# Performance work log

Hardware: AMD Instinct MI355X
Metric: run time of the kernel (lower is better)

Reference implementation:

```python
import jax, jax.numpy as jnp
import numpy as np

B, S, E, H = 2, 2048, 1024, 16
D = E // H  # head_dim = 64


def setup_inputs() -> dict:
    key = jax.random.key(0)
    k1, k2, k3 = jax.random.split(key, 3)
    scale = 0.02  # GPT-2 init scale
    return {
        "hidden_states": jax.random.normal(k1, (B, S, E), dtype=jnp.float32),
        "c_attn_w": jax.random.normal(k2, (E, 3 * E), dtype=jnp.float32) * scale,
        "c_attn_b": jnp.zeros((3 * E,), dtype=jnp.float32),
        "c_proj_w": jax.random.normal(k3, (E, E), dtype=jnp.float32) * scale,
        "c_proj_b": jnp.zeros((E,), dtype=jnp.float32),
    }


def reference(hidden_states, c_attn_w, c_attn_b, c_proj_w, c_proj_b):
    # Conv1D: x @ W + b  -> qkv [B, S, 3E]
    qkv = hidden_states @ c_attn_w + c_attn_b
    q, k, v = jnp.split(qkv, 3, axis=-1)

    # split heads -> [B, H, S, D]
    def split_heads(t):
        return t.reshape(B, S, H, D).transpose(0, 2, 1, 3)

    q, k, v = split_heads(q), split_heads(k), split_heads(v)

    # naive full attention: QK^T / sqrt(D) -> softmax -> @ V
    attn_weights = jnp.einsum("bhqd,bhkd->bhqk", q, k) / jnp.sqrt(
        jnp.asarray(D, dtype=q.dtype)
    )
    attn_weights = jax.nn.softmax(attn_weights, axis=-1)
    attn_output = jnp.einsum("bhqk,bhkd->bhqd", attn_weights, v)

    # merge heads -> [B, S, E], then output projection
    attn_output = attn_output.transpose(0, 2, 1, 3).reshape(B, S, E)
    attn_output = attn_output @ c_proj_w + c_proj_b
    return attn_output
```

## Files before the change

### kernel.cpp

```cpp
#include <hip/hip_runtime.h>

#define SEQ 2048
#define EMB 1024
#define KDIM 1024
#define CF 0.180336880111113f

typedef __attribute__((ext_vector_type(8))) short short8_t;
typedef __attribute__((ext_vector_type(4))) float floatx4;
typedef __attribute__((ext_vector_type(4))) unsigned short ushort4_t;
typedef __attribute__((ext_vector_type(4))) unsigned int uivec4;

#define GLOAD16(gp, lp)                                                        \
  __builtin_amdgcn_global_load_lds(                                            \
      (const __attribute__((address_space(1))) void*)(gp),                     \
      (__attribute__((address_space(3))) void*)(lp), 16, 0, 0)

#define WGBAR()                                   \
  do {                                            \
    __asm__ __volatile__("" ::: "memory");        \
    __builtin_amdgcn_s_barrier();                 \
    __asm__ __volatile__("" ::: "memory");        \
  } while (0)

static __device__ __forceinline__ unsigned short f2bf(float x) {
  unsigned int u = __float_as_uint(x);
  return (unsigned short)((u + 0x7fffu + ((u >> 16) & 1u)) >> 16);
}

static __device__ __forceinline__ short8_t mk_pb(unsigned int a, unsigned int b,
                                                 unsigned int c, unsigned int d) {
  uivec4 t;
  t[0] = a; t[1] = b; t[2] = c; t[3] = d;
  return __builtin_bit_cast(short8_t, t);
}

static __device__ __forceinline__ unsigned int pack_bf(float p0, float p1) {
  return __builtin_amdgcn_perm(__float_as_uint(p1), __float_as_uint(p0),
                               0x07060302u);
}

static __device__ __forceinline__ void tconv_tile(
    const float* __restrict__ W, unsigned short* __restrict__ T, int N, int K,
    int n0, int k0, int tid) {
  __shared__ float Tl[64][65];
  const int lx = tid & 15, ly = tid >> 4;
#pragma unroll
  for (int u = 0; u < 4; ++u) {
    int r = u * 16 + ly;
    float4 v = *(const float4*)&W[(size_t)(k0 + r) * N + n0 + lx * 4];
    Tl[r][lx * 4 + 0] = v.x;
    Tl[r][lx * 4 + 1] = v.y;
    Tl[r][lx * 4 + 2] = v.z;
    Tl[r][lx * 4 + 3] = v.w;
  }
  __syncthreads();
#pragma unroll
  for (int u = 0; u < 4; ++u) {
    int n = u * 16 + ly;
    ushort4_t h;
#pragma unroll
    for (int v = 0; v < 4; ++v) h[v] = f2bf(Tl[lx * 4 + v][n]);
    *(ushort4_t*)&T[(size_t)(n0 + n) * K + k0 + lx * 4] = h;
  }
}

__global__ __launch_bounds__(256) void prep(
    const float* __restrict__ hs, const float* __restrict__ caw,
    const float* __restrict__ cpw, unsigned short* __restrict__ hsb,
    unsigned short* __restrict__ w1t, unsigned short* __restrict__ w2t) {
  const int bid = blockIdx.x, tid = threadIdx.x;
  if (bid < 4096) {
    const int i = bid * 256 + tid;
    float4 v = *(const float4*)&hs[(size_t)i * 4];
    ushort4_t h = {f2bf(v.x), f2bf(v.y), f2bf(v.z), f2bf(v.w)};
    *(ushort4_t*)&hsb[(size_t)i * 4] = h;
  } else if (bid < 4864) {
    const int idx = bid - 4096;
    tconv_tile(caw, w1t, 3 * EMB, EMB, (idx % 48) * 64, (idx / 48) * 64, tid);
  } else {
    const int idx = bid - 4864;
    tconv_tile(cpw, w2t, EMB, EMB, (idx % 16) * 64, (idx / 16) * 64, tid);
  }
}

template <int MODE, int BN>
__global__ __launch_bounds__(256, 4) void gemm_pl(
    const unsigned short* __restrict__ Ag, const unsigned short* __restrict__ Bg,
    const float* __restrict__ bias, float* __restrict__ outF,
    unsigned short* __restrict__ qk, unsigned short* __restrict__ vt) {
  __shared__ __attribute__((aligned(16))) unsigned short Ah[2][128 * 32];
  __shared__ __attribute__((aligned(16))) unsigned short Bh[2][BN * 32];
  const int NJ = BN / 32;

  const int tid = threadIdx.x;
  const int w = tid >> 6, lane = tid & 63;
  const int quad = lane >> 4, c = lane & 15;

  int bm, bn;
  {
    const int L = blockIdx.x, x = L & 7, g = L >> 3;
    if (MODE == 0) {
      bm = ((x & 1) * 16 + (g & 15)) * 128;
      bn = ((x >> 1) * 6 + (g >> 4)) * 128;
    } else {
      bm = ((x & 3) * 8 + (g & 7)) * 128;
      bn = ((x >> 2) * 8 + (g >> 3)) * 64;
    }
  }
  const int wm = (w >> 1) * 64, wn = (w & 1) * (BN / 2);

  const unsigned short* gsrc = (w < 2) ? Ag : Bg;
  const int lbo = (w < 2) ? (w & 1) * 64 * 32 : (w & 1) * (BN / 2) * 32;
  const int rbase = (w < 2) ? (bm + (w & 1) * 64) : (bn + (w & 1) * (BN / 2));
  const int nloads = (w < 2) ? 4 : (BN / 32);
  const int srow = lane >> 2;
  const int sblk = (lane & 3) ^ ((lane >> 3) & 3);
  const char* gp0 = (const char*)(gsrc + (size_t)(rbase + srow) * KDIM) + sblk * 16;

  floatx4 acc[4][NJ];
  const floatx4 z = {0.f, 0.f, 0.f, 0.f};
#pragma unroll
  for (int i = 0; i < 4; ++i)
#pragma unroll
    for (int j = 0; j < NJ; ++j) acc[i][j] = z;

  const int sw = (c >> 1) & 3;

#define STAGE_G(buf, kt)                                                       \
  do {                                                                         \
    unsigned short* ld = ((w < 2) ? Ah[buf] : Bh[buf]) + lbo;                  \
    const char* gp = gp0 + (size_t)(kt) * 64;                                  \
    for (int i_ = 0; i_ < nloads; ++i_)                                        \
      GLOAD16(gp + (size_t)i_ * 16 * (KDIM * 2), &ld[i_ * 512]);               \
  } while (0)

  STAGE_G(0, 0);

  for (int t = 0; t < 32; ++t) {
    __asm__ __volatile__("s_waitcnt vmcnt(0)" ::: "memory");
    WGBAR();
    if (t < 31) STAGE_G((t + 1) & 1, t + 1);
    const unsigned short* Ac = Ah[t & 1];
    const unsigned short* Bc = Bh[t & 1];

    const int oct = (quad ^ sw) * 8;
    short8_t a[4], b[NJ];
#pragma unroll
    for (int i = 0; i < 4; ++i)
      a[i] = *(const short8_t*)&Ac[(wm + 16 * i + c) * 32 + oct];
#pragma unroll
    for (int j = 0; j < NJ; ++j)
      b[j] = *(const short8_t*)&Bc[(wn + 16 * j + c) * 32 + oct];
#pragma unroll
    for (int i = 0; i < 4; ++i)
#pragma unroll
      for (int j = 0; j < NJ; ++j)
        acc[i][j] = __builtin_amdgcn_mfma_f32_16x16x32_bf16(b[j], a[i], acc[i][j], 0, 0, 0);
  }
#undef STAGE_G

#pragma unroll
  for (int i = 0; i < 4; ++i) {
    const int row = bm + wm + 16 * i + c;
#pragma unroll
    for (int j = 0; j < NJ; ++j) {
      const int col0 = bn + wn + 16 * j + quad * 4;
      floatx4 v = acc[i][j] + *(const floatx4*)&bias[col0];
      if (MODE == 0) {
        if (col0 < 1024) v = v * CF;
        if (col0 < 2048) {
          ushort4_t pk = {f2bf(v[0]), f2bf(v[1]), f2bf(v[2]), f2bf(v[3])};
          *(ushort4_t*)&qk[(size_t)row * 2048 + col0] = pk;
        } else {
          const int c2 = col0 - 2048, hh = c2 >> 6, d0 = c2 & 63;
          const int bb = row >> 11, s = row & 2047;
          const int j = s & 63;
          const int lam = (j & 0x20) | ((j & 0x0C) << 1) | ((j & 0x10) >> 2) | (j & 3);
          const int sp = (s & ~63) | lam;
          unsigned short* vb = &vt[((size_t)(bb * 16 + hh) * 64 + d0) * 2048 + sp];
          vb[0 * 2048] = f2bf(v[0]);
          vb[1 * 2048] = f2bf(v[1]);
          vb[2 * 2048] = f2bf(v[2]);
          vb[3 * 2048] = f2bf(v[3]);
        }
      } else {
        *(floatx4*)&outF[(size_t)row * 1024 + col0] = v;
      }
    }
  }
}

static __device__ __forceinline__ void stage_kv16(
    int w, int srow, int sblkg, const unsigned short* __restrict__ gK,
    const unsigned short* __restrict__ gV, unsigned short* Kbuf,
    unsigned short* Vbuf, int jt) {
  if (w < 4) {
    const unsigned short* g0 =
        gK + (size_t)(jt * 64 + w * 16 + srow) * 2048 + sblkg * 8;
    unsigned short* l0 = &Kbuf[(w * 16) * 64];
    GLOAD16(g0, l0);
    GLOAD16(g0 + (size_t)8 * 2048, l0 + 8 * 64);
  } else {
    const unsigned short* g0 =
        gV + (size_t)((w - 4) * 16 + srow) * 2048 + jt * 64 + sblkg * 8;
    unsigned short* l0 = &Vbuf[((w - 4) * 16) * 64];
    GLOAD16(g0, l0);
    GLOAD16(g0 + (size_t)8 * 2048, l0 + 8 * 64);
  }
}

__global__ __launch_bounds__(512, 1) void attn10(
    const unsigned short* __restrict__ qk, const unsigned short* __restrict__ vt,
    unsigned short* __restrict__ ao) {
  __shared__ __attribute__((aligned(16))) unsigned short KV[6 * 4096];
  unsigned short* Ksb = KV;
  unsigned short* Vsb = KV + 3 * 4096;

  const int tid = threadIdx.x;
  const int w = tid >> 6, lane = tid & 63, quad = lane >> 4, c = lane & 15;
  const int qh = w >> 1, kh = w & 1;
  const int L = blockIdx.x, x = L & 7, g = L >> 3;
  const int hb = x * 4 + (g >> 3);
  const int h = hb & 15, b = hb >> 4;
  const int q0 = (g & 7) * 256;
  const int rk = c & 7;

  short8_t qf[4][2];
  {
    const size_t rb = (size_t)b * SEQ + q0 + qh * 64;
#pragma unroll
    for (int mi = 0; mi < 4; ++mi) {
      const size_t qr = (rb + mi * 16 + c) * 2048 + h * 64 + quad * 8;
      qf[mi][0] = *(const short8_t*)&qk[qr];
      qf[mi][1] = *(const short8_t*)&qk[qr + 32];
    }
  }
  __asm__ __volatile__("s_waitcnt vmcnt(0)" ::: "memory");

  floatx4 O[4][4], Osum[4];
  const floatx4 z = {0.f, 0.f, 0.f, 0.f};
#pragma unroll
  for (int mi = 0; mi < 4; ++mi) {
    Osum[mi] = z;
#pragma unroll
    for (int dg = 0; dg < 4; ++dg) O[mi][dg] = z;
  }
  short8_t ones;
#pragma unroll
  for (int e = 0; e < 8; ++e) ones[e] = (short)0x3F80;

  const int srow = lane >> 3;
  const int sblkg = (lane & 7) ^ srow;
  const unsigned short* gK = qk + (size_t)b * SEQ * 2048 + 1024 + h * 64;
  const unsigned short* gV = vt + (size_t)(b * 16 + h) * 64 * 2048;

  stage_kv16(w, srow, sblkg, gK, gV, Ksb, Vsb, 0);
  stage_kv16(w, srow, sblkg, gK, gV, Ksb + 4096, Vsb + 4096, 1);

  const int octv = ((4 * kh + quad) ^ rk) * 8;

  for (int t = 0; t < 32; ++t) {
    __asm__ __volatile__("s_waitcnt vmcnt(2)" ::: "memory");
    WGBAR();
    stage_kv16(w, srow, sblkg, gK, gV, Ksb + ((t + 2) % 3) * 4096,
               Vsb + ((t + 2) % 3) * 4096, (t + 2) & 31);
    const unsigned short* Kc = Ksb + (t % 3) * 4096;
    const unsigned short* Vc = Vsb + (t % 3) * 4096;

    floatx4 S[4][2];
#pragma unroll
    for (int mi = 0; mi < 4; ++mi)
#pragma unroll
      for (int jg = 0; jg < 2; ++jg) S[mi][jg] = z;
#pragma unroll
    for (int kd = 0; kd < 2; ++kd) {
      const int oct = ((4 * kd + quad) ^ rk) * 8;
#pragma unroll
      for (int jg = 0; jg < 2; ++jg) {
        short8_t kf = *(const short8_t*)&Kc[((kh * 2 + jg) * 16 + c) * 64 + oct];
#pragma unroll
        for (int mi = 0; mi < 4; ++mi)
          S[mi][jg] = __builtin_amdgcn_mfma_f32_16x16x32_bf16(kf, qf[mi][kd], S[mi][jg], 0, 0, 0);
      }
    }

#pragma unroll
    for (int mi = 0; mi < 4; ++mi) {
      unsigned int pw[2][2];
#pragma unroll
      for (int jg = 0; jg < 2; ++jg) {
        float p0 = __builtin_amdgcn_exp2f(S[mi][jg][0]);
        float p1 = __builtin_amdgcn_exp2f(S[mi][jg][1]);
        float p2 = __builtin_amdgcn_exp2f(S[mi][jg][2]);
        float p3 = __builtin_amdgcn_exp2f(S[mi][jg][3]);
        pw[jg][0] = pack_bf(p0, p1);
        pw[jg][1] = pack_bf(p2, p3);
      }
      short8_t pb = mk_pb(pw[0][0], pw[0][1], pw[1][0], pw[1][1]);
      Osum[mi] = __builtin_amdgcn_mfma_f32_16x16x32_bf16(ones, pb, Osum[mi], 0, 0, 0);
#pragma unroll
      for (int dg = 0; dg < 4; ++dg) {
        short8_t vf = *(const short8_t*)&Vc[(dg * 16 + c) * 64 + octv];
        O[mi][dg] = __builtin_amdgcn_mfma_f32_16x16x32_bf16(vf, pb, O[mi][dg], 0, 0, 0);
      }
    }
  }

  __asm__ __volatile__("s_waitcnt vmcnt(0)" ::: "memory");
  WGBAR();

  float* Of = (float*)KV;
  float* Ss2 = (float*)((char*)KV + 34816);
#pragma unroll
  for (int p = 0; p < 2; ++p) {
    if (kh == 1 && (qh >> 1) == p) {
#pragma unroll
      for (int mi = 0; mi < 4; ++mi) {
        const int row = (qh & 1) * 64 + mi * 16 + c;
        float* orow = &Of[row * 68];
#pragma unroll
        for (int dg = 0; dg < 4; ++dg)
          *(floatx4*)&orow[dg * 16 + quad * 4] = O[mi][dg];
        if (quad == 0) Ss2[row] = Osum[mi][0];
      }
    }
    WGBAR();
    if (kh == 0 && (qh >> 1) == p) {
#pragma unroll
      for (int mi = 0; mi < 4; ++mi) {
        const int row = (qh & 1) * 64 + mi * 16 + c;
        const float inv = 1.0f / (Osum[mi][0] + Ss2[row]);
        const float* orow = &Of[row * 68];
        const size_t grow = (size_t)b * SEQ + q0 + qh * 64 + mi * 16 + c;
#pragma unroll
        for (int dg = 0; dg < 4; ++dg) {
          floatx4 o = O[mi][dg] + *(const floatx4*)&orow[dg * 16 + quad * 4];
          ushort4_t ov = {f2bf(o[0] * inv), f2bf(o[1] * inv),
                          f2bf(o[2] * inv), f2bf(o[3] * inv)};
          *(ushort4_t*)&ao[grow * EMB + h * 64 + dg * 16 + quad * 4] = ov;
        }
      }
    }
    WGBAR();
  }
}

extern "C" void kernel_launch(void* const* d_in, const int* in_sizes, int n_in,
                              void* d_out, int out_size, void* d_ws, size_t ws_size,
                              hipStream_t stream) {
  const float* hs = (const float*)d_in[0];
  const float* c_attn_w = (const float*)d_in[1];
  const float* c_attn_b = (const float*)d_in[2];
  const float* c_proj_w = (const float*)d_in[3];
  const float* c_proj_b = (const float*)d_in[4];
  float* out = (float*)d_out;

  char* ws = (char*)d_ws;
  unsigned short* hsb = (unsigned short*)(ws + 0);
  unsigned short* qk  = (unsigned short*)(ws + 8388608);
  unsigned short* vt  = (unsigned short*)(ws + 25165824);
  unsigned short* aob = (unsigned short*)(ws + 33554432);
  unsigned short* w1t = (unsigned short*)(ws + 41943040);
  unsigned short* w2t = (unsigned short*)(ws + 48234496);

  prep<<<5120, 256, 0, stream>>>(hs, c_attn_w, c_proj_w, hsb, w1t, w2t);
  gemm_pl<0, 128><<<768, 256, 0, stream>>>(hsb, w1t, c_attn_b, nullptr, qk, vt);
  attn10<<<256, 512, 0, stream>>>(qk, vt, aob);
  gemm_pl<2, 64><<<512, 256, 0, stream>>>(aob, w2t, c_proj_b, out, nullptr, nullptr);
}
```

Before: 175.8 us.

## Double K-step depth in GEMMs and KV tile size in attention

The GEMM kernels now stage 64-wide K slices instead of 32 (16 iterations instead of 32), using an XOR swizzle over 8 blocks, with launch bounds lowered to match the larger LDS use. The attention kernel processes 128 keys per iteration instead of 64. Each wave now covers 64 keys, and the V tile is split across two sub-buffers in a triple-buffered ring. The aim is to halve barrier and wait overhead per unit of work and raise MFMA density per iteration. The cost is more LDS and registers per block, which lowers occupancy.

```diff
diff --git a/kernel.cpp b/kernel.cpp
--- a/kernel.cpp
+++ b/kernel.cpp
@@ -84,17 +84,18 @@
 }
 
 template <int MODE, int BN>
-__global__ __launch_bounds__(256, 4) void gemm_pl(
+__global__ __launch_bounds__(256, MODE == 0 ? 2 : 3) void gemm_pl(
     const unsigned short* __restrict__ Ag, const unsigned short* __restrict__ Bg,
     const float* __restrict__ bias, float* __restrict__ outF,
     unsigned short* __restrict__ qk, unsigned short* __restrict__ vt) {
-  __shared__ __attribute__((aligned(16))) unsigned short Ah[2][128 * 32];
-  __shared__ __attribute__((aligned(16))) unsigned short Bh[2][BN * 32];
+  __shared__ __attribute__((aligned(16))) unsigned short Ah[2][128 * 64];
+  __shared__ __attribute__((aligned(16))) unsigned short Bh[2][BN * 64];
   const int NJ = BN / 32;
 
   const int tid = threadIdx.x;
   const int w = tid >> 6, lane = tid & 63;
   const int quad = lane >> 4, c = lane & 15;
+  const int rk = c & 7;
 
   int bm, bn;
   {
@@ -110,12 +111,12 @@
   const int wm = (w >> 1) * 64, wn = (w & 1) * (BN / 2);
 
   const unsigned short* gsrc = (w < 2) ? Ag : Bg;
-  const int lbo = (w < 2) ? (w & 1) * 64 * 32 : (w & 1) * (BN / 2) * 32;
+  const int lbo = (w < 2) ? (w & 1) * 64 * 64 : (w & 1) * (BN / 2) * 64;
   const int rbase = (w < 2) ? (bm + (w & 1) * 64) : (bn + (w & 1) * (BN / 2));
-  const int nloads = (w < 2) ? 4 : (BN / 32);
-  const int srow = lane >> 2;
-  const int sblk = (lane & 3) ^ ((lane >> 3) & 3);
-  const char* gp0 = (const char*)(gsrc + (size_t)(rbase + srow) * KDIM) + sblk * 16;
+  const int nloads = (w < 2) ? 8 : (BN / 16);
+  const int srow = lane >> 3;
+  const int sblkg = (lane & 7) ^ srow;
+  const char* gp0 = (const char*)(gsrc + (size_t)(rbase + srow) * KDIM) + sblkg * 16;
 
   floatx4 acc[4][NJ];
   const floatx4 z = {0.f, 0.f, 0.f, 0.f};
@@ -123,39 +124,40 @@
   for (int i = 0; i < 4; ++i)
 #pragma unroll
     for (int j = 0; j < NJ; ++j) acc[i][j] = z;
-
-  const int sw = (c >> 1) & 3;
 
 #define STAGE_G(buf, kt)                                                       \
   do {                                                                         \
     unsigned short* ld = ((w < 2) ? Ah[buf] : Bh[buf]) + lbo;                  \
-    const char* gp = gp0 + (size_t)(kt) * 64;                                  \
+    const char* gp = gp0 + (size_t)(kt) * 128;                                 \
     for (int i_ = 0; i_ < nloads; ++i_)                                        \
-      GLOAD16(gp + (size_t)i_ * 16 * (KDIM * 2), &ld[i_ * 512]);               \
+      GLOAD16(gp + (size_t)i_ * 8 * (KDIM * 2), &ld[i_ * 512]);                \
   } while (0)
 
   STAGE_G(0, 0);
 
-  for (int t = 0; t < 32; ++t) {
+  for (int t = 0; t < 16; ++t) {
     __asm__ __volatile__("s_waitcnt vmcnt(0)" ::: "memory");
     WGBAR();
-    if (t < 31) STAGE_G((t + 1) & 1, t + 1);
+    if (t < 15) STAGE_G((t + 1) & 1, t + 1);
     const unsigned short* Ac = Ah[t & 1];
     const unsigned short* Bc = Bh[t & 1];
 
-    const int oct = (quad ^ sw) * 8;
-    short8_t a[4], b[NJ];
-#pragma unroll
-    for (int i = 0; i < 4; ++i)
-      a[i] = *(const short8_t*)&Ac[(wm + 16 * i + c) * 32 + oct];
-#pragma unroll
-    for (int j = 0; j < NJ; ++j)
-      b[j] = *(const short8_t*)&Bc[(wn + 16 * j + c) * 32 + oct];
-#pragma unroll
-    for (int i = 0; i < 4; ++i)
+#pragma unroll
+    for (int kd = 0; kd < 2; ++kd) {
+      const int oct = ((4 * kd + quad) ^ rk) * 8;
+      short8_t a[4], b[NJ];
+#pragma unroll
+      for (int i = 0; i < 4; ++i)
+        a[i] = *(const short8_t*)&Ac[(wm + 16 * i + c) * 64 + oct];
 #pragma unroll
       for (int j = 0; j < NJ; ++j)
-        acc[i][j] = __builtin_amdgcn_mfma_f32_16x16x32_bf16(b[j], a[i], acc[i][j], 0, 0, 0);
+        b[j] = *(const short8_t*)&Bc[(wn + 16 * j + c) * 64 + oct];
+#pragma unroll
+      for (int i = 0; i < 4; ++i)
+#pragma unroll
+        for (int j = 0; j < NJ; ++j)
+          acc[i][j] = __builtin_amdgcn_mfma_f32_16x16x32_bf16(b[j], a[i], acc[i][j], 0, 0, 0);
+    }
   }
 #undef STAGE_G
 
@@ -190,31 +192,33 @@
   }
 }
 
-static __device__ __forceinline__ void stage_kv16(
+static __device__ __forceinline__ void stage_kv128(
     int w, int srow, int sblkg, const unsigned short* __restrict__ gK,
     const unsigned short* __restrict__ gV, unsigned short* Kbuf,
     unsigned short* Vbuf, int jt) {
   if (w < 4) {
     const unsigned short* g0 =
-        gK + (size_t)(jt * 64 + w * 16 + srow) * 2048 + sblkg * 8;
-    unsigned short* l0 = &Kbuf[(w * 16) * 64];
-    GLOAD16(g0, l0);
-    GLOAD16(g0 + (size_t)8 * 2048, l0 + 8 * 64);
+        gK + (size_t)(jt * 128 + w * 32 + srow) * 2048 + sblkg * 8;
+    unsigned short* l0 = &Kbuf[(w * 32) * 64];
+#pragma unroll
+    for (int i = 0; i < 4; ++i) GLOAD16(g0 + (size_t)i * 8 * 2048, &l0[i * 512]);
   } else {
+    const int sub = (w - 4) >> 1;
+    const int dh = ((w - 4) & 1) * 32;
     const unsigned short* g0 =
-        gV + (size_t)((w - 4) * 16 + srow) * 2048 + jt * 64 + sblkg * 8;
-    unsigned short* l0 = &Vbuf[((w - 4) * 16) * 64];
-    GLOAD16(g0, l0);
-    GLOAD16(g0 + (size_t)8 * 2048, l0 + 8 * 64);
-  }
-}
-
-__global__ __launch_bounds__(512, 1) void attn10(
+        gV + (size_t)(dh + srow) * 2048 + jt * 128 + sub * 64 + sblkg * 8;
+    unsigned short* l0 = &Vbuf[sub * 4096 + dh * 64];
+#pragma unroll
+    for (int i = 0; i < 4; ++i) GLOAD16(g0 + (size_t)i * 8 * 2048, &l0[i * 512]);
+  }
+}
+
+__global__ __launch_bounds__(512, 1) void attn11(
     const unsigned short* __restrict__ qk, const unsigned short* __restrict__ vt,
     unsigned short* __restrict__ ao) {
-  __shared__ __attribute__((aligned(16))) unsigned short KV[6 * 4096];
+  __shared__ __attribute__((aligned(16))) unsigned short KV[48 * 1024];
   unsigned short* Ksb = KV;
-  unsigned short* Vsb = KV + 3 * 4096;
+  unsigned short* Vsb = KV + 3 * 8192;
 
   const int tid = threadIdx.x;
   const int w = tid >> 6, lane = tid & 63, quad = lane >> 4, c = lane & 15;
@@ -254,41 +258,40 @@
   const unsigned short* gK = qk + (size_t)b * SEQ * 2048 + 1024 + h * 64;
   const unsigned short* gV = vt + (size_t)(b * 16 + h) * 64 * 2048;
 
-  stage_kv16(w, srow, sblkg, gK, gV, Ksb, Vsb, 0);
-  stage_kv16(w, srow, sblkg, gK, gV, Ksb + 4096, Vsb + 4096, 1);
-
-  const int octv = ((4 * kh + quad) ^ rk) * 8;
-
-  for (int t = 0; t < 32; ++t) {
-    __asm__ __volatile__("s_waitcnt vmcnt(2)" ::: "memory");
+  stage_kv128(w, srow, sblkg, gK, gV, Ksb, Vsb, 0);
+  stage_kv128(w, srow, sblkg, gK, gV, Ksb + 8192, Vsb + 8192, 1);
+
+  for (int t = 0; t < 16; ++t) {
+    __asm__ __volatile__("s_waitcnt vmcnt(4)" ::: "memory");
     WGBAR();
-    stage_kv16(w, srow, sblkg, gK, gV, Ksb + ((t + 2) % 3) * 4096,
-               Vsb + ((t + 2) % 3) * 4096, (t + 2) & 31);
-    const unsigned short* Kc = Ksb + (t % 3) * 4096;
-    const unsigned short* Vc = Vsb + (t % 3) * 4096;
-
-    floatx4 S[4][2];
+    stage_kv128(w, srow, sblkg, gK, gV, Ksb + ((t + 2) % 3) * 8192,
+                Vsb + ((t + 2) % 3) * 8192, (t + 2) & 15);
+    const unsigned short* Kc = Ksb + (t % 3) * 8192 + kh * 64 * 64;
+    const unsigned short* Vc = Vsb + (t % 3) * 8192 + kh * 4096;
+
+    floatx4 S[4][4];
 #pragma unroll
     for (int mi = 0; mi < 4; ++mi)
 #pragma unroll
-      for (int jg = 0; jg < 2; ++jg) S[mi][jg] = z;
+      for (int jg = 0; jg < 4; ++jg) S[mi][jg] = z;
 #pragma unroll
     for (int kd = 0; kd < 2; ++kd) {
       const int oct = ((4 * kd + quad) ^ rk) * 8;
 #pragma unroll
-      for (int jg = 0; jg < 2; ++jg) {
-        short8_t kf = *(const short8_t*)&Kc[((kh * 2 + jg) * 16 + c) * 64 + oct];
+      for (int jg = 0; jg < 4; ++jg) {
+        short8_t kf = *(const short8_t*)&Kc[(jg * 16 + c) * 64 + oct];
 #pragma unroll
         for (int mi = 0; mi < 4; ++mi)
           S[mi][jg] = __builtin_amdgcn_mfma_f32_16x16x32_bf16(kf, qf[mi][kd], S[mi][jg], 0, 0, 0);
       }
     }
 
+    short8_t pbA[4], pbB[4];
 #pragma unroll
     for (int mi = 0; mi < 4; ++mi) {
-      unsigned int pw[2][2];
-#pragma unroll
-      for (int jg = 0; jg < 2; ++jg) {
+      unsigned int pw[4][2];
+#pragma unroll
+      for (int jg = 0; jg < 4; ++jg) {
         float p0 = __builtin_amdgcn_exp2f(S[mi][jg][0]);
         float p1 = __builtin_amdgcn_exp2f(S[mi][jg][1]);
         float p2 = __builtin_amdgcn_exp2f(S[mi][jg][2]);
@@ -296,12 +299,22 @@
         pw[jg][0] = pack_bf(p0, p1);
         pw[jg][1] = pack_bf(p2, p3);
       }
-      short8_t pb = mk_pb(pw[0][0], pw[0][1], pw[1][0], pw[1][1]);
-      Osum[mi] = __builtin_amdgcn_mfma_f32_16x16x32_bf16(ones, pb, Osum[mi], 0, 0, 0);
+      pbA[mi] = mk_pb(pw[0][0], pw[0][1], pw[1][0], pw[1][1]);
+      pbB[mi] = mk_pb(pw[2][0], pw[2][1], pw[3][0], pw[3][1]);
+      Osum[mi] = __builtin_amdgcn_mfma_f32_16x16x32_bf16(ones, pbA[mi], Osum[mi], 0, 0, 0);
+      Osum[mi] = __builtin_amdgcn_mfma_f32_16x16x32_bf16(ones, pbB[mi], Osum[mi], 0, 0, 0);
+    }
+
+#pragma unroll
+    for (int kq = 0; kq < 2; ++kq) {
+      const int octv = ((4 * kq + quad) ^ rk) * 8;
 #pragma unroll
       for (int dg = 0; dg < 4; ++dg) {
         short8_t vf = *(const short8_t*)&Vc[(dg * 16 + c) * 64 + octv];
-        O[mi][dg] = __builtin_amdgcn_mfma_f32_16x16x32_bf16(vf, pb, O[mi][dg], 0, 0, 0);
+#pragma unroll
+        for (int mi = 0; mi < 4; ++mi)
+          O[mi][dg] = __builtin_amdgcn_mfma_f32_16x16x32_bf16(
+              vf, kq ? pbB[mi] : pbA[mi], O[mi][dg], 0, 0, 0);
       }
     }
   }
@@ -365,6 +378,6 @@
 
   prep<<<5120, 256, 0, stream>>>(hs, c_attn_w, c_proj_w, hsb, w1t, w2t);
   gemm_pl<0, 128><<<768, 256, 0, stream>>>(hsb, w1t, c_attn_b, nullptr, qk, vt);
-  attn10<<<256, 512, 0, stream>>>(qk, vt, aob);
+  attn11<<<256, 512, 0, stream>>>(qk, vt, aob);
   gemm_pl<2, 64><<<512, 256, 0, stream>>>(aob, w2t, c_proj_b, out, nullptr, nullptr);
 }
```

Measured after the change: 169.2 us. 1.04x faster.
